# Kernel optimization log

Measured on AMD Instinct MI355X. Metric: run time of the kernel, lower is better.

## Reference

```python
import jax, jax.numpy as jnp
from jax import lax
import numpy as np

NUM_CLASSES = 6
WIN = 11


def setup_inputs() -> dict:
    key = jax.random.key(0)
    k1, k2 = jax.random.split(key)
    x = jax.random.normal(k1, (8, NUM_CLASSES, 512, 512), dtype=jnp.float32)
    target = jax.random.randint(k2, (8, 1, 512, 512), 0, NUM_CLASSES, dtype=jnp.int32)
    return {"x": x, "target": target}


def reference(x, target):
    # log-softmax over class dim
    log_p = jax.nn.log_softmax(x, axis=1)  # [B,C,H,W]

    w = -jnp.ones((1, 1, WIN, WIN), dtype=jnp.float32)
    w = w.at[0, 0, WIN // 2, WIN // 2].set(float(WIN * WIN - 1))
    t = target.astype(jnp.float32)  # [B,1,H,W]
    edge = lax.conv_general_dilated(
        t, w, window_strides=(1, 1), padding='SAME',
        dimension_numbers=('NCHW', 'OIHW', 'NCHW'))
    edge_mask = (edge != 0).astype(jnp.float32)  # [B,1,H,W], binarized

    # dynamic smoothing = fraction of edge pixels, capped at 0.2
    s = jnp.minimum(jnp.mean(edge_mask), jnp.float32(0.2))

    labels = target[:, 0]  # [B,H,W]
    onehot = jax.nn.one_hot(labels, NUM_CLASSES, axis=1, dtype=jnp.float32)  # [B,C,H,W]
    # to_categorical(alpha=s): alpha off-class, 1 - alpha + alpha/C on-class
    soft = s * (1.0 - onehot) + (1.0 - s + s / NUM_CLASSES) * onehot

    mask = onehot * (1.0 - edge_mask) + soft * edge_mask  # [B,C,H,W]
    loss = jnp.mean(jnp.sum(mask * log_p, axis=1))
    return -loss
```

## Files before the change

kernel.cpp:

```cpp
#include <hip/hip_runtime.h>

#define BATCH   8
#define NCLS    6
#define HW      512
#define IMGPIX  (HW * HW)
#define NPIX    (BATCH * IMGPIX)
#define TILE    32
#define HALO    5
#define SM      (TILE + 2 * HALO)
#define RSTRIDE 36
#define NB      (BATCH * 256)

__device__ __forceinline__ float get4(const float4& v, int j) {
    return j == 0 ? v.x : j == 1 ? v.y : j == 2 ? v.z : v.w;
}

__global__ __launch_bounds__(256, 4) void ls_main_kernel(
        const float* __restrict__ x,
        const int*   __restrict__ tgt,
        float*       __restrict__ part) {
    __shared__ int   s_t[SM][SM];
    __shared__ int   s_rs[SM][RSTRIDE];
    __shared__ float sw1[4], sw2[4];
    __shared__ int   swe[4];

    const int tid  = threadIdx.x;
    const int blk  = blockIdx.x;
    const int b    = blk >> 8;
    const int tile = blk & 255;
    const int tr   = (tile >> 4) * TILE;
    const int tc   = (tile & 15) * TILE;

    const int* timg = tgt + b * IMGPIX;

    int tv[7];
#pragma unroll
    for (int i = 0; i < 7; i++) {
        const int e  = tid + i * 256;
        const int ly = (e * 1560) >> 16;
        const int lx = e - ly * SM;
        int v = 0;
        if (e < SM * SM) {
            const int gy = tr - HALO + ly, gx = tc - HALO + lx;
            if (gy >= 0 && gy < HW && gx >= 0 && gx < HW) v = timg[gy * HW + gx];
        }
        tv[i] = v;
    }

    const int p0 = tid * 4;
    const int py = p0 >> 5;
    const int px = p0 & 31;
    const int gy = tr + py;
    const int gx = tc + px;
    const float* xb = x + ((size_t)(b * NCLS) << 18) + (size_t)gy * HW + gx;
    float4 xc[NCLS];
#pragma unroll
    for (int c = 0; c < NCLS; c++)
        xc[c] = *(const float4*)(xb + ((size_t)c << 18));

#pragma unroll
    for (int i = 0; i < 7; i++) {
        const int e  = tid + i * 256;
        if (e < SM * SM) {
            const int ly = (e * 1560) >> 16;
            const int lx = e - ly * SM;
            s_t[ly][lx] = tv[i];
        }
    }
    __syncthreads();

    for (int e = tid; e < SM * TILE; e += 256) {
        const int ry = e >> 5, cx = e & 31;
        int s = 0;
#pragma unroll
        for (int dx = 0; dx <= 2 * HALO; dx++) s += s_t[ry][cx + dx];
        s_rs[ry][cx] = s;
    }
    __syncthreads();

    int4 bs = make_int4(0, 0, 0, 0);
#pragma unroll
    for (int dy = 0; dy <= 2 * HALO; dy++) {
        const int4 r = *(const int4*)&s_rs[py + dy][px];
        bs.x += r.x; bs.y += r.y; bs.z += r.z; bs.w += r.w;
    }
    const int bsa[4] = {bs.x, bs.y, bs.z, bs.w};
    int t4[4];
#pragma unroll
    for (int j = 0; j < 4; j++) t4[j] = s_t[py + HALO][px + HALO + j];

    float r1 = 0.f, r2 = 0.f;
    int ec = 0;
#pragma unroll
    for (int j = 0; j < 4; j++) {
        const float a0 = get4(xc[0], j), a1 = get4(xc[1], j), a2 = get4(xc[2], j);
        const float a3 = get4(xc[3], j), a4 = get4(xc[4], j), a5 = get4(xc[5], j);
        const float m  = fmaxf(fmaxf(fmaxf(a0, a1), fmaxf(a2, a3)), fmaxf(a4, a5));
        const float se = __expf(a0 - m) + __expf(a1 - m) + __expf(a2 - m) +
                         __expf(a3 - m) + __expf(a4 - m) + __expf(a5 - m);
        const float lse = m + __logf(se);
        const int   t   = t4[j];
        const float xt  = t == 0 ? a0 : t == 1 ? a1 : t == 2 ? a2 :
                          t == 3 ? a3 : t == 4 ? a4 : a5;
        const float lpl = xt - lse;
        r1 += lpl;
        const int ev = 121 * t - bsa[j];
        const int eb = (ev != 0) ? 1 : 0;
        const float S = (a0 + a1 + a2 + a3 + a4 + a5) - 6.f * lse;
        r2 = fmaf((float)eb, S - (11.0f / 6.0f) * lpl, r2);
        ec += eb;
    }

#pragma unroll
    for (int off = 32; off > 0; off >>= 1) {
        r1 += __shfl_down(r1, off);
        r2 += __shfl_down(r2, off);
        ec += __shfl_down(ec, off);
    }
    const int wave = tid >> 6;
    if ((tid & 63) == 0) { sw1[wave] = r1; sw2[wave] = r2; swe[wave] = ec; }
    __syncthreads();
    if (tid == 0) {
        part[blk]          = sw1[0] + sw1[1] + sw1[2] + sw1[3];
        part[NB + blk]     = sw2[0] + sw2[1] + sw2[2] + sw2[3];
        part[2 * NB + blk] = (float)(swe[0] + swe[1] + swe[2] + swe[3]);
    }
}

__global__ __launch_bounds__(256) void ls_finalize_kernel(
        const float* __restrict__ part,
        float* __restrict__ out) {
    const int tid = threadIdx.x;
    double d1 = 0.0, d2 = 0.0, de = 0.0;
#pragma unroll
    for (int i = 0; i < NB / 256; i++) {
        const int idx = tid + i * 256;
        d1 += (double)part[idx];
        d2 += (double)part[NB + idx];
        de += (double)part[2 * NB + idx];
    }
#pragma unroll
    for (int off = 32; off > 0; off >>= 1) {
        d1 += __shfl_down(d1, off);
        d2 += __shfl_down(d2, off);
        de += __shfl_down(de, off);
    }
    __shared__ double sd1[4], sd2[4], sde[4];
    const int wave = tid >> 6;
    if ((tid & 63) == 0) { sd1[wave] = d1; sd2[wave] = d2; sde[wave] = de; }
    __syncthreads();
    if (tid == 0) {
        const double R1 = sd1[0] + sd1[1] + sd1[2] + sd1[3];
        const double R2 = sd2[0] + sd2[1] + sd2[2] + sd2[3];
        const double E  = sde[0] + sde[1] + sde[2] + sde[3];
        const float  s  = fminf((float)E * (1.0f / (float)NPIX), 0.2f);
        const double loss = (R1 + (double)s * R2) * (1.0 / (double)NPIX);
        out[0] = (float)(-loss);
    }
}

extern "C" void kernel_launch(void* const* d_in, const int* in_sizes, int n_in,
                              void* d_out, int out_size, void* d_ws, size_t ws_size,
                              hipStream_t stream) {
    const float* x   = (const float*)d_in[0];
    const int*   tgt = (const int*)d_in[1];
    float*       out = (float*)d_out;
    float*       part = (float*)d_ws;

    ls_main_kernel<<<NB, 256, 0, stream>>>(x, tgt, part);
    ls_finalize_kernel<<<1, 256, 0, stream>>>(part, out);
}
```

Before: 92.88 us.

## Interleave batch in block order, sliding-window row sums, drop softmax max

```diff
diff --git a/kernel.cpp b/kernel.cpp
--- a/kernel.cpp
+++ b/kernel.cpp
@@ -19,15 +19,15 @@
         const float* __restrict__ x,
         const int*   __restrict__ tgt,
         float*       __restrict__ part) {
-    __shared__ int   s_t[SM][SM];
+    __shared__ int   s_t[SM * SM];
     __shared__ int   s_rs[SM][RSTRIDE];
     __shared__ float sw1[4], sw2[4];
     __shared__ int   swe[4];
 
     const int tid  = threadIdx.x;
     const int blk  = blockIdx.x;
-    const int b    = blk >> 8;
-    const int tile = blk & 255;
+    const int b    = blk & 7;
+    const int tile = blk >> 3;
     const int tr   = (tile >> 4) * TILE;
     const int tc   = (tile & 15) * TILE;
 
@@ -37,7 +37,7 @@
 #pragma unroll
     for (int i = 0; i < 7; i++) {
         const int e  = tid + i * 256;
-        const int ly = (e * 1560) >> 16;
+        const int ly = e / SM;
         const int lx = e - ly * SM;
         int v = 0;
         if (e < SM * SM) {
@@ -47,12 +47,11 @@
         tv[i] = v;
     }
 
-    const int p0 = tid * 4;
-    const int py = p0 >> 5;
-    const int px = p0 & 31;
+    const int py = tid >> 3;
+    const int px = (tid & 7) << 2;
     const int gy = tr + py;
     const int gx = tc + px;
-    const float* xb = x + ((size_t)(b * NCLS) << 18) + (size_t)gy * HW + gx;
+    const float* xb = x + ((size_t)(b * NCLS) << 18) + (gy << 9) + gx;
     float4 xc[NCLS];
 #pragma unroll
     for (int c = 0; c < NCLS; c++)
@@ -60,21 +59,27 @@
 
 #pragma unroll
     for (int i = 0; i < 7; i++) {
-        const int e  = tid + i * 256;
-        if (e < SM * SM) {
-            const int ly = (e * 1560) >> 16;
-            const int lx = e - ly * SM;
-            s_t[ly][lx] = tv[i];
-        }
+        const int e = tid + i * 256;
+        if (e < SM * SM) s_t[e] = tv[i];
     }
     __syncthreads();
 
-    for (int e = tid; e < SM * TILE; e += 256) {
-        const int ry = e >> 5, cx = e & 31;
-        int s = 0;
+    if (tid < SM * 4) {
+        const int row  = tid >> 2;
+        const int c0   = (tid & 3) << 3;
+        const int base = row * SM + c0;
+        int buf[18];
 #pragma unroll
-        for (int dx = 0; dx <= 2 * HALO; dx++) s += s_t[ry][cx + dx];
-        s_rs[ry][cx] = s;
+        for (int k = 0; k < 18; k++) buf[k] = s_t[base + k];
+        int acc = 0;
+#pragma unroll
+        for (int k = 0; k < 11; k++) acc += buf[k];
+        s_rs[row][c0] = acc;
+#pragma unroll
+        for (int k = 1; k < 8; k++) {
+            acc += buf[k + 10] - buf[k - 1];
+            s_rs[row][c0 + k] = acc;
+        }
     }
     __syncthreads();
 
@@ -87,7 +92,7 @@
     const int bsa[4] = {bs.x, bs.y, bs.z, bs.w};
     int t4[4];
 #pragma unroll
-    for (int j = 0; j < 4; j++) t4[j] = s_t[py + HALO][px + HALO + j];
+    for (int j = 0; j < 4; j++) t4[j] = s_t[(py + HALO) * SM + px + HALO + j];
 
     float r1 = 0.f, r2 = 0.f;
     int ec = 0;
@@ -95,10 +100,9 @@
     for (int j = 0; j < 4; j++) {
         const float a0 = get4(xc[0], j), a1 = get4(xc[1], j), a2 = get4(xc[2], j);
         const float a3 = get4(xc[3], j), a4 = get4(xc[4], j), a5 = get4(xc[5], j);
-        const float m  = fmaxf(fmaxf(fmaxf(a0, a1), fmaxf(a2, a3)), fmaxf(a4, a5));
-        const float se = __expf(a0 - m) + __expf(a1 - m) + __expf(a2 - m) +
-                         __expf(a3 - m) + __expf(a4 - m) + __expf(a5 - m);
-        const float lse = m + __logf(se);
+        const float se = __expf(a0) + __expf(a1) + __expf(a2) +
+                         __expf(a3) + __expf(a4) + __expf(a5);
+        const float lse = __logf(se);
         const int   t   = t4[j];
         const float xt  = t == 0 ? a0 : t == 1 ? a1 : t == 2 ? a2 :
                           t == 3 ? a3 : t == 4 ? a4 : a5;
```

After: 89.45 us. -3.7%, faster.
